# Performance work log

Hardware: AMD Instinct MI355X
Metric: run time of the kernel (lower is better)

Reference implementation:

```python
import jax, jax.numpy as jnp
import numpy as np

T, HID, HQ, HKV, D = 2048, 4096, 32, 8, 128
ROPE_BASE = 10000.0


def setup_inputs() -> dict:
    key = jax.random.key(0)
    ks = jax.random.split(key, 5)
    scale = 0.02
    hidden_states = jax.random.normal(ks[0], (T, HID), dtype=jnp.float32)
    position_ids = jnp.arange(T, dtype=jnp.int32)
    # HF-style rotary tables: freqs duplicated along last dim -> [T, D]
    inv_freq = 1.0 / (ROPE_BASE ** (jnp.arange(0, D, 2, dtype=jnp.float32) / D))
    ang = position_ids.astype(jnp.float32)[:, None] * inv_freq[None, :]  # [T, D/2]
    emb = jnp.concatenate([ang, ang], axis=-1)  # [T, D]
    cos, sin = jnp.cos(emb), jnp.sin(emb)
    Wq = jax.random.normal(ks[1], (HID, HQ * D), dtype=jnp.float32) * scale
    Wk = jax.random.normal(ks[2], (HID, HKV * D), dtype=jnp.float32) * scale
    Wv = jax.random.normal(ks[3], (HID, HKV * D), dtype=jnp.float32) * scale
    Wo = jax.random.normal(ks[4], (HQ * D, HID), dtype=jnp.float32) * scale
    return {"hidden_states": hidden_states, "position_ids": position_ids,
            "cos": cos, "sin": sin, "Wq": Wq, "Wk": Wk, "Wv": Wv, "Wo": Wo}


def _rotate_half(x):
    x1, x2 = jnp.split(x, 2, axis=-1)
    return jnp.concatenate([-x2, x1], axis=-1)


def reference(hidden_states, position_ids, cos, sin, Wq, Wk, Wv, Wo):
    t = hidden_states.shape[0]
    scaling = D ** -0.5
    # QKV projections (attention_bias=False)
    q = (hidden_states @ Wq).reshape(t, HQ, D)   # [T, Hq, D]
    k = (hidden_states @ Wk).reshape(t, HKV, D)  # [T, Hkv, D]
    v = (hidden_states @ Wv).reshape(t, HKV, D)
    # RoPE: cos/sin [T, D] broadcast over heads
    c, s = cos[:, None, :], sin[:, None, :]
    q = q * c + _rotate_half(q) * s
    k = k * c + _rotate_half(k) * s
    # GQA: expand KV heads to query heads
    groups = HQ // HKV
    k = jnp.repeat(k, groups, axis=1)  # [T, Hq, D]
    v = jnp.repeat(v, groups, axis=1)
    # Causal attention
    scores = jnp.einsum('thd,shd->hts', q, k) * scaling  # [Hq, T, T]
    causal = jnp.tril(jnp.ones((t, t), dtype=bool))
    scores = jnp.where(causal[None], scores, jnp.finfo(scores.dtype).min)
    probs = jax.nn.softmax(scores, axis=-1)
    attn = jnp.einsum('hts,shd->thd', probs, v).reshape(t, HQ * D)
    return attn @ Wo
```

## Files before the change

### kernel.cpp

```cpp
#include <hip/hip_runtime.h>
#include <hip/hip_bf16.h>
#include <cstdint>
#include <cstddef>

#define T_DIM   2048
#define HID     4096
#define HQ      32
#define HKV     8
#define D_HEAD  128
#define QKV_N   6144
#define KOFF    4096
#define VOFF    5120

typedef __attribute__((ext_vector_type(8))) short short8;
typedef __attribute__((ext_vector_type(4))) float floatx4;

__device__ __forceinline__ ushort f2bf(float f) {
    union { float f; uint u; } v; v.f = f;
    uint r = v.u + 0x7fffu + ((v.u >> 16) & 1u);
    return (ushort)(r >> 16);
}
__device__ __forceinline__ float bf2f(ushort h) {
    union { uint u; float f; } v; v.u = ((uint)h) << 16; return v.f;
}
__device__ __forceinline__ short8 ld8(const ushort* p) {
    uint2 a = *(const uint2*)p, b = *(const uint2*)(p + 4);
    union { uint u[4]; short8 s; } x;
    x.u[0] = a.x; x.u[1] = a.y; x.u[2] = b.x; x.u[3] = b.y;
    return x.s;
}
__device__ __forceinline__ void gld_lds16(const ushort* g, ushort* l) {
    __builtin_amdgcn_global_load_lds(
        (__attribute__((address_space(1))) void*)(g),
        (__attribute__((address_space(3))) void*)(l), 16, 0, 0);
}

__global__ void cast_f32_bf16(const float* __restrict__ in, ushort* __restrict__ out, int n) {
    int i = (blockIdx.x * blockDim.x + threadIdx.x) * 4;
    if (i < n) {
        float4 v = *(const float4*)(in + i);
        ushort4 o;
        o.x = f2bf(v.x); o.y = f2bf(v.y); o.z = f2bf(v.z); o.w = f2bf(v.w);
        *(ushort4*)(out + i) = o;
    }
}

__global__ __launch_bounds__(256) void transpose_cast(const float* __restrict__ W,
                                                      ushort* __restrict__ Wt, int K, int N) {
    __shared__ ushort tile[64][66];
    int n0 = blockIdx.x * 64, k0 = blockIdx.y * 64;
    int tx = threadIdx.x & 15, ty = threadIdx.x >> 4;
#pragma unroll
    for (int i = 0; i < 4; i++) {
        int r = ty + i * 16;
        float4 v = *(const float4*)&W[(size_t)(k0 + r) * N + n0 + tx * 4];
        tile[tx * 4 + 0][r] = f2bf(v.x);
        tile[tx * 4 + 1][r] = f2bf(v.y);
        tile[tx * 4 + 2][r] = f2bf(v.z);
        tile[tx * 4 + 3][r] = f2bf(v.w);
    }
    __syncthreads();
#pragma unroll
    for (int i = 0; i < 4; i++) {
        int nr = ty + i * 16;
        ushort4 o = *(const ushort4*)&tile[nr][tx * 4];
        *(ushort4*)&Wt[(size_t)(n0 + nr) * K + k0 + tx * 4] = o;
    }
}

__global__ void transpose_v(const ushort* __restrict__ qkv, ushort* __restrict__ VtG) {
    __shared__ ushort tile[32][33];
    int t0 = blockIdx.x * 32, d0 = blockIdx.y * 32, kvh = blockIdx.z;
    int tx = threadIdx.x & 31, ty = threadIdx.x >> 5;
#pragma unroll
    for (int i = 0; i < 4; i++) {
        int t = t0 + ty + i * 8;
        tile[ty + i * 8][tx] = qkv[(size_t)t * QKV_N + VOFF + kvh * D_HEAD + d0 + tx];
    }
    __syncthreads();
#pragma unroll
    for (int i = 0; i < 4; i++) {
        int d = d0 + ty + i * 8;
        VtG[((size_t)kvh * D_HEAD + d) * T_DIM + t0 + tx] = tile[tx][ty + i * 8];
    }
}

template <typename OutT>
__global__ __launch_bounds__(512, 2) void gemm256(const ushort* __restrict__ A,
                                                  const ushort* __restrict__ Bt,
                                                  OutT* __restrict__ C,
                                                  int K, int lda, int ldb, int ldc) {
    __shared__ ushort As[2][16384];
    __shared__ ushort Bs[2][16384];
    int tid = threadIdx.x;
    int wid = tid >> 6, lane = tid & 63, quad = lane >> 4, l15 = lane & 15;
    int wr = wid >> 2, wc = wid & 3;
    int bh = wc >> 1, br = (wc & 1) * 64;
    int m0 = blockIdx.x * 256, n0 = blockIdx.y * 256;
    int sw = (l15 & 7);

    floatx4 acc[8][4];
    floatx4 z = {0.f, 0.f, 0.f, 0.f};
#pragma unroll
    for (int i = 0; i < 8; i++)
#pragma unroll
        for (int j = 0; j < 4; j++) acc[i][j] = z;

    int NT = K >> 6;

    int r8 = tid >> 3;
    int csw = (tid & 7) ^ (r8 & 7);
    const ushort* sA = A  + (size_t)(m0 + r8) * lda + csw * 8;
    const ushort* sB = Bt + (size_t)(n0 + r8) * ldb + csw * 8;

    gld_lds16(sA,                          &As[0][tid * 8]);
    gld_lds16(sA + (size_t)128 * lda,      &As[0][8192 + tid * 8]);
    gld_lds16(sB,                          &Bs[0][tid * 8]);
    gld_lds16(sB + (size_t)128 * ldb,      &Bs[0][8192 + tid * 8]);
    gld_lds16(sB + (size_t)64 * ldb,       &Bs[0][4096 + tid * 8]);
    gld_lds16(sB + (size_t)192 * ldb,      &Bs[0][12288 + tid * 8]);
    gld_lds16(sA + (size_t)64 * lda,       &As[0][4096 + tid * 8]);
    gld_lds16(sA + (size_t)192 * lda,      &As[0][12288 + tid * 8]);
    asm volatile("s_waitcnt vmcnt(2)" ::: "memory");
    __builtin_amdgcn_sched_barrier(0);
    __builtin_amdgcn_s_barrier();

    short8 bfr[4][2];
    short8 af[2][2];

    for (int t = 0; t < NT; ++t) {
        int slot = t & 1, ns = slot ^ 1;
        const ushort* tA = &As[slot][wr * 8192];
        const ushort* tB = &Bs[slot][bh * 8192];
        size_t ko = (size_t)(t + 1) * 64;
        bool pf = (t + 1 < NT);

#pragma unroll
        for (int nf = 0; nf < 4; ++nf)
#pragma unroll
            for (int kh = 0; kh < 2; ++kh)
                bfr[nf][kh] = *(const short8*)&tB[(br + nf * 16 + l15) * 64 +
                                                  (((quad + kh * 4) ^ sw) * 8)];
#pragma unroll
        for (int mi = 0; mi < 2; ++mi)
#pragma unroll
            for (int kh = 0; kh < 2; ++kh)
                af[mi][kh] = *(const short8*)&tA[(mi * 16 + l15) * 64 +
                                                 (((quad + kh * 4) ^ sw) * 8)];
        if (pf) {
            gld_lds16(sA + ko,                     &As[ns][tid * 8]);
            gld_lds16(sA + (size_t)128 * lda + ko, &As[ns][8192 + tid * 8]);
        }
        __builtin_amdgcn_sched_barrier(0);
        __builtin_amdgcn_s_barrier();
        asm volatile("s_waitcnt lgkmcnt(0)" ::: "memory");
        __builtin_amdgcn_sched_barrier(0);
        __builtin_amdgcn_s_setprio(1);
#pragma unroll
        for (int nf = 0; nf < 4; ++nf)
#pragma unroll
            for (int mi = 0; mi < 2; ++mi)
#pragma unroll
                for (int kh = 0; kh < 2; ++kh)
                    acc[mi][nf] = __builtin_amdgcn_mfma_f32_16x16x32_bf16(af[mi][kh], bfr[nf][kh], acc[mi][nf], 0, 0, 0);
        __builtin_amdgcn_s_setprio(0);
        __builtin_amdgcn_sched_barrier(0);
        __builtin_amdgcn_s_barrier();

#pragma unroll
        for (int mi = 0; mi < 2; ++mi)
#pragma unroll
            for (int kh = 0; kh < 2; ++kh)
                af[mi][kh] = *(const short8*)&tA[(32 + mi * 16 + l15) * 64 +
                                                 (((quad + kh * 4) ^ sw) * 8)];
        if (pf) {
            gld_lds16(sB + ko,                     &Bs[ns][tid * 8]);
            gld_lds16(sB + (size_t)128 * ldb + ko, &Bs[ns][8192 + tid * 8]);
        }
        __builtin_amdgcn_sched_barrier(0);
        __builtin_amdgcn_s_barrier();
        asm volatile("s_waitcnt lgkmcnt(0)" ::: "memory");
        __builtin_amdgcn_sched_barrier(0);
        __builtin_amdgcn_s_setprio(1);
#pragma unroll
        for (int nf = 0; nf < 4; ++nf)
#pragma unroll
            for (int mi = 0; mi < 2; ++mi)
#pragma unroll
                for (int kh = 0; kh < 2; ++kh)
                    acc[2 + mi][nf] = __builtin_amdgcn_mfma_f32_16x16x32_bf16(af[mi][kh], bfr[nf][kh], acc[2 + mi][nf], 0, 0, 0);
        __builtin_amdgcn_s_setprio(0);
        __builtin_amdgcn_sched_barrier(0);
        if (pf) asm volatile("s_waitcnt vmcnt(4)" ::: "memory");
        else    asm volatile("s_waitcnt vmcnt(0)" ::: "memory");
        __builtin_amdgcn_sched_barrier(0);
        __builtin_amdgcn_s_barrier();

#pragma unroll
        for (int mi = 0; mi < 2; ++mi)
#pragma unroll
            for (int kh = 0; kh < 2; ++kh)
                af[mi][kh] = *(const short8*)&tA[(64 + mi * 16 + l15) * 64 +
                                                 (((quad + kh * 4) ^ sw) * 8)];
        if (pf) {
            gld_lds16(sB + (size_t)64 * ldb + ko,  &Bs[ns][4096 + tid * 8]);
            gld_lds16(sB + (size_t)192 * ldb + ko, &Bs[ns][12288 + tid * 8]);
        }
        __builtin_amdgcn_sched_barrier(0);
        __builtin_amdgcn_s_barrier();
        asm volatile("s_waitcnt lgkmcnt(0)" ::: "memory");
        __builtin_amdgcn_sched_barrier(0);
        __builtin_amdgcn_s_setprio(1);
#pragma unroll
        for (int nf = 0; nf < 4; ++nf)
#pragma unroll
            for (int mi = 0; mi < 2; ++mi)
#pragma unroll
                for (int kh = 0; kh < 2; ++kh)
                    acc[4 + mi][nf] = __builtin_amdgcn_mfma_f32_16x16x32_bf16(af[mi][kh], bfr[nf][kh], acc[4 + mi][nf], 0, 0, 0);
        __builtin_amdgcn_s_setprio(0);
        __builtin_amdgcn_sched_barrier(0);
        __builtin_amdgcn_s_barrier();

#pragma unroll
        for (int mi = 0; mi < 2; ++mi)
#pragma unroll
            for (int kh = 0; kh < 2; ++kh)
                af[mi][kh] = *(const short8*)&tA[(96 + mi * 16 + l15) * 64 +
                                                 (((quad + kh * 4) ^ sw) * 8)];
        if (pf) {
            gld_lds16(sA + (size_t)64 * lda + ko,  &As[ns][4096 + tid * 8]);
            gld_lds16(sA + (size_t)192 * lda + ko, &As[ns][12288 + tid * 8]);
        }
        __builtin_amdgcn_sched_barrier(0);
        __builtin_amdgcn_s_barrier();
        asm volatile("s_waitcnt lgkmcnt(0)" ::: "memory");
        __builtin_amdgcn_sched_barrier(0);
        __builtin_amdgcn_s_setprio(1);
#pragma unroll
        for (int nf = 0; nf < 4; ++nf)
#pragma unroll
            for (int mi = 0; mi < 2; ++mi)
#pragma unroll
                for (int kh = 0; kh < 2; ++kh)
                    acc[6 + mi][nf] = __builtin_amdgcn_mfma_f32_16x16x32_bf16(af[mi][kh], bfr[nf][kh], acc[6 + mi][nf], 0, 0, 0);
        __builtin_amdgcn_s_setprio(0);
        __builtin_amdgcn_sched_barrier(0);
        if (pf) asm volatile("s_waitcnt vmcnt(2)" ::: "memory");
        __builtin_amdgcn_sched_barrier(0);
        __builtin_amdgcn_s_barrier();
    }

#pragma unroll
    for (int i = 0; i < 8; ++i) {
        int row0 = m0 + wr * 128 + i * 16 + quad * 4;
#pragma unroll
        for (int j = 0; j < 4; ++j) {
            int col = n0 + wc * 64 + j * 16 + l15;
#pragma unroll
            for (int r = 0; r < 4; ++r) {
                float v = acc[i][j][r];
                if constexpr (sizeof(OutT) == 2)
                    C[(size_t)(row0 + r) * ldc + col] = (OutT)f2bf(v);
                else
                    C[(size_t)(row0 + r) * ldc + col] = v;
            }
        }
    }
}

template <typename OutT>
__global__ __launch_bounds__(256) void gemm_bt(const ushort* __restrict__ A,
                                               const ushort* __restrict__ Bt,
                                               OutT* __restrict__ C,
                                               int K, int lda, int ldb, int ldc) {
    __shared__ ushort As[2][128 * 32];
    __shared__ ushort Bs[2][128 * 32];
    int tid = threadIdx.x;
    int w = tid >> 6, lane = tid & 63, quad = lane >> 4, l15 = lane & 15;
    int wr = (w >> 1) * 64, wc = (w & 1) * 64;
    int m0 = blockIdx.x * 128, n0 = blockIdx.y * 128;

    floatx4 acc[4][4];
    floatx4 z = {0.f, 0.f, 0.f, 0.f};
#pragma unroll
    for (int i = 0; i < 4; i++)
#pragma unroll
        for (int j = 0; j < 4; j++) acc[i][j] = z;

    int arow = tid >> 2, ac = (tid & 3) * 8;
    const ushort* gA0 = A + (size_t)(m0 + arow) * lda + ac;
    const ushort* gA1 = A + (size_t)(m0 + arow + 64) * lda + ac;
    const ushort* gB0 = Bt + (size_t)(n0 + arow) * ldb + ac;
    const ushort* gB1 = Bt + (size_t)(n0 + arow + 64) * ldb + ac;

    gld_lds16(gA0, &As[0][tid * 8]);
    gld_lds16(gA1, &As[0][64 * 32 + tid * 8]);
    gld_lds16(gB0, &Bs[0][tid * 8]);
    gld_lds16(gB1, &Bs[0][64 * 32 + tid * 8]);
    gA0 += 32; gA1 += 32; gB0 += 32; gB1 += 32;

    int cur = 0;
    for (int k0 = 0; k0 < K; k0 += 32, cur ^= 1) {
        __syncthreads();
        if (k0 + 32 < K) {
            gld_lds16(gA0, &As[cur ^ 1][tid * 8]);
            gld_lds16(gA1, &As[cur ^ 1][64 * 32 + tid * 8]);
            gld_lds16(gB0, &Bs[cur ^ 1][tid * 8]);
            gld_lds16(gB1, &Bs[cur ^ 1][64 * 32 + tid * 8]);
            gA0 += 32; gA1 += 32; gB0 += 32; gB1 += 32;
        }

        short8 af[4];
#pragma unroll
        for (int i = 0; i < 4; i++)
            af[i] = *(const short8*)&As[cur][(wr + i * 16 + l15) * 32 + quad * 8];
#pragma unroll
        for (int j = 0; j < 4; j++) {
            short8 bf = *(const short8*)&Bs[cur][(wc + j * 16 + l15) * 32 + quad * 8];
#pragma unroll
            for (int i = 0; i < 4; i++)
                acc[i][j] = __builtin_amdgcn_mfma_f32_16x16x32_bf16(af[i], bf, acc[i][j], 0, 0, 0);
        }
    }

#pragma unroll
    for (int i = 0; i < 4; i++) {
        int row0 = m0 + wr + i * 16 + quad * 4;
#pragma unroll
        for (int j = 0; j < 4; j++) {
            int col = n0 + wc + j * 16 + l15;
#pragma unroll
            for (int r = 0; r < 4; r++) {
                float v = acc[i][j][r];
                if constexpr (sizeof(OutT) == 2)
                    C[(size_t)(row0 + r) * ldc + col] = (OutT)f2bf(v);
                else
                    C[(size_t)(row0 + r) * ldc + col] = v;
            }
        }
    }
}

__global__ void rope_kernel(ushort* __restrict__ qkv, const float* __restrict__ cosb,
                            const float* __restrict__ sinb) {
    int t = blockIdx.x;
    ushort* row = qkv + (size_t)t * QKV_N;
    const float* cr = cosb + (size_t)t * D_HEAD;
    const float* sr = sinb + (size_t)t * D_HEAD;
    for (int c = threadIdx.x; c < 2560; c += 256) {
        int slice = c >> 6, d = c & 63;
        int col = slice * 128 + d;
        float x0 = bf2f(row[col]), x1 = bf2f(row[col + 64]);
        float cs = cr[d], sn = sr[d];
        row[col] = f2bf(x0 * cs - x1 * sn);
        row[col + 64] = f2bf(x1 * cs + x0 * sn);
    }
}

#define PS_STRIDE 68

__global__ __launch_bounds__(256, 2) void attn_kernel(const ushort* __restrict__ qkv,
                                                      const ushort* __restrict__ VtG,
                                                      ushort* __restrict__ attn) {
    __shared__ ushort Ks[64 * 128];
    __shared__ ushort Vt[128 * 64];
    __shared__ ushort Ps[128 * PS_STRIDE];

    int qt = (gridDim.x - 1) - blockIdx.x;
    int h = blockIdx.y;
    int q0 = qt * 128;
    int kbmax = 2 * qt + 1;
    int tid = threadIdx.x, w = tid >> 6, lane = tid & 63, quad = lane >> 4, l15 = lane & 15;
    int kvh = h >> 2;

    const ushort* kbase = qkv + (size_t)KOFF + (size_t)kvh * D_HEAD;
    const ushort* vbase = VtG + (size_t)kvh * D_HEAD * T_DIM;

    const ushort* ksrc[4];
    const ushort* vsrc[4];
#pragma unroll
    for (int i = 0; i < 4; i++) {
        int cid = i * 256 + tid;
        int kr = cid >> 4, kp = cid & 15, kc = kp ^ (kr & 15);
        ksrc[i] = kbase + (size_t)kr * QKV_N + kc * 8;
        int vr = cid >> 3, vp = cid & 7, vc = vp ^ (vr & 7);
        vsrc[i] = vbase + (size_t)vr * T_DIM + vc * 8;
    }

#pragma unroll
    for (int i = 0; i < 4; i++) {
        gld_lds16(ksrc[i], &Ks[(i * 256 + tid) * 8]);
        ksrc[i] += (size_t)64 * QKV_N;
    }

    short8 qf[2][4];
#pragma unroll
    for (int s = 0; s < 2; s++) {
        const ushort* qrow = qkv + (size_t)(q0 + s * 64 + w * 16 + l15) * QKV_N + h * D_HEAD + quad * 8;
#pragma unroll
        for (int ks = 0; ks < 4; ks++)
            qf[s][ks] = *(const short8*)(qrow + ks * 32);
    }

    floatx4 o[2][8];
    floatx4 z = {0.f, 0.f, 0.f, 0.f};
#pragma unroll
    for (int s = 0; s < 2; s++)
#pragma unroll
        for (int j = 0; j < 8; j++) o[s][j] = z;
    float lsum[2][4] = {{0.f, 0.f, 0.f, 0.f}, {0.f, 0.f, 0.f, 0.f}};

    const float scale_l2e = 0.08838834764831845f * 1.4426950408889634f;
    const float BOUND = 24.0f;

    __syncthreads();

    for (int kb = 0; kb <= kbmax; kb++) {
        bool act0 = (kb <= 2 * qt);

#pragma unroll
        for (int i = 0; i < 4; i++) {
            gld_lds16(vsrc[i], &Vt[(i * 256 + tid) * 8]);
            vsrc[i] += 64;
        }

        floatx4 sc[2][4];
#pragma unroll
        for (int s = 0; s < 2; s++)
#pragma unroll
            for (int jt = 0; jt < 4; jt++) sc[s][jt] = z;
#pragma unroll
        for (int ks = 0; ks < 4; ks++) {
#pragma unroll
            for (int jt = 0; jt < 4; jt++) {
                short8 kf = ld8(&Ks[(jt * 16 + l15) * 128 + (((ks * 4 + quad) ^ l15) * 8)]);
                if (act0)
                    sc[0][jt] = __builtin_amdgcn_mfma_f32_16x16x32_bf16(qf[0][ks], kf, sc[0][jt], 0, 0, 0);
                sc[1][jt] = __builtin_amdgcn_mfma_f32_16x16x32_bf16(qf[1][ks], kf, sc[1][jt], 0, 0, 0);
            }
        }

#pragma unroll
        for (int s = 0; s < 2; s++) {
            if (s == 0 && !act0) continue;
            bool diag = (kb == 2 * qt + s);
#pragma unroll
            for (int r = 0; r < 4; r++) {
                int rloc = w * 16 + quad * 4 + r;
#pragma unroll
                for (int jt = 0; jt < 4; jt++) {
                    float v = fmaf(sc[s][jt][r], scale_l2e, -BOUND);
                    if (diag && (jt * 16 + l15 > rloc)) v = -1e30f;
                    float p = exp2f(v);
                    lsum[s][r] += p;
                    Ps[(s * 64 + rloc) * PS_STRIDE + jt * 16 + l15] = f2bf(p);
                }
            }
        }

        __syncthreads();

        if (kb < kbmax) {
#pragma unroll
            for (int i = 0; i < 4; i++) {
                gld_lds16(ksrc[i], &Ks[(i * 256 + tid) * 8]);
                ksrc[i] += (size_t)64 * QKV_N;
            }
        }

#pragma unroll
        for (int ks2 = 0; ks2 < 2; ks2++) {
            short8 pf0 = ld8(&Ps[(w * 16 + l15) * PS_STRIDE + ks2 * 32 + quad * 8]);
            short8 pf1 = ld8(&Ps[(64 + w * 16 + l15) * PS_STRIDE + ks2 * 32 + quad * 8]);
#pragma unroll
            for (int jt = 0; jt < 8; jt++) {
                short8 vf = ld8(&Vt[(jt * 16 + l15) * 64 + (((ks2 * 4 + quad) ^ (l15 & 7)) * 8)]);
                if (act0)
                    o[0][jt] = __builtin_amdgcn_mfma_f32_16x16x32_bf16(pf0, vf, o[0][jt], 0, 0, 0);
                o[1][jt] = __builtin_amdgcn_mfma_f32_16x16x32_bf16(pf1, vf, o[1][jt], 0, 0, 0);
            }
        }

        __syncthreads();
    }

#pragma unroll
    for (int s = 0; s < 2; s++) {
#pragma unroll
        for (int r = 0; r < 4; r++) {
            float l = lsum[s][r];
#pragma unroll
            for (int mk = 1; mk <= 8; mk <<= 1) l += __shfl_xor(l, mk);
            float inv = 1.f / l;
            int trow = q0 + s * 64 + w * 16 + quad * 4 + r;
            ushort* orow = attn + (size_t)trow * (HQ * D_HEAD) + h * D_HEAD;
#pragma unroll
            for (int jt = 0; jt < 8; jt++)
                orow[jt * 16 + l15] = f2bf(o[s][jt][r] * inv);
        }
    }
}

extern "C" void kernel_launch(void* const* d_in, const int* in_sizes, int n_in,
                              void* d_out, int out_size, void* d_ws, size_t ws_size,
                              hipStream_t stream) {
    const float* hidden = (const float*)d_in[0];
    const float* cosb = (const float*)d_in[2];
    const float* sinb = (const float*)d_in[3];
    const float* Wq = (const float*)d_in[4];
    const float* Wk = (const float*)d_in[5];
    const float* Wv = (const float*)d_in[6];
    const float* Wo = (const float*)d_in[7];
    float* out = (float*)d_out;

    char* ws = (char*)d_ws;
    ushort* hiddenB = (ushort*)(ws);
    ushort* WqkvT   = (ushort*)(ws + (size_t)(16u << 20));
    ushort* WoT     = (ushort*)(ws + (size_t)(64u << 20));
    ushort* qkv     = (ushort*)(ws + (size_t)(96u << 20));
    ushort* attnO   = (ushort*)(ws + (size_t)(120u << 20));
    ushort* VtG     = (ushort*)(ws + (size_t)(136u << 20));

    cast_f32_bf16<<<8192, 256, 0, stream>>>(hidden, hiddenB, T_DIM * HID);
    transpose_cast<<<dim3(64, 64), 256, 0, stream>>>(Wq, WqkvT, HID, 4096);
    transpose_cast<<<dim3(16, 64), 256, 0, stream>>>(Wk, WqkvT + (size_t)4096 * HID, HID, 1024);
    transpose_cast<<<dim3(16, 64), 256, 0, stream>>>(Wv, WqkvT + (size_t)5120 * HID, HID, 1024);
    transpose_cast<<<dim3(64, 64), 256, 0, stream>>>(Wo, WoT, HID, 4096);

    gemm256<ushort><<<dim3(8, 24), 512, 0, stream>>>(hiddenB, WqkvT, qkv,
                                                     HID, HID, HID, QKV_N);
    rope_kernel<<<T_DIM, 256, 0, stream>>>(qkv, cosb, sinb);
    transpose_v<<<dim3(64, 4, 8), 256, 0, stream>>>(qkv, VtG);
    attn_kernel<<<dim3(T_DIM / 128, HQ), 256, 0, stream>>>(qkv, VtG, attnO);
    gemm_bt<float><<<dim3(16, 32), 256, 0, stream>>>(attnO, WoT, out,
                                                     HID, HID, HID, HID);
}
```

Baseline: 569.8 us.

## Retile QKV and output GEMMs for full CU coverage, vectorize rope and transpose

```diff
diff --git a/kernel.cpp b/kernel.cpp
--- a/kernel.cpp
+++ b/kernel.cpp
@@ -47,7 +47,7 @@
 
 __global__ __launch_bounds__(256) void transpose_cast(const float* __restrict__ W,
                                                       ushort* __restrict__ Wt, int K, int N) {
-    __shared__ ushort tile[64][66];
+    __shared__ ushort tile[64][72];
     int n0 = blockIdx.x * 64, k0 = blockIdx.y * 64;
     int tx = threadIdx.x & 15, ty = threadIdx.x >> 4;
 #pragma unroll
@@ -61,10 +61,11 @@
     }
     __syncthreads();
 #pragma unroll
-    for (int i = 0; i < 4; i++) {
-        int nr = ty + i * 16;
-        ushort4 o = *(const ushort4*)&tile[nr][tx * 4];
-        *(ushort4*)&Wt[(size_t)(n0 + nr) * K + k0 + tx * 4] = o;
+    for (int i = 0; i < 2; i++) {
+        int task = i * 256 + threadIdx.x;
+        int nr = task >> 3, c = task & 7;
+        short8 o = *(const short8*)&tile[nr][c * 8];
+        *(short8*)&Wt[(size_t)(n0 + nr) * K + k0 + c * 8] = o;
     }
 }
 
@@ -85,71 +86,67 @@
     }
 }
 
-template <typename OutT>
-__global__ __launch_bounds__(512, 2) void gemm256(const ushort* __restrict__ A,
-                                                  const ushort* __restrict__ Bt,
-                                                  OutT* __restrict__ C,
-                                                  int K, int lda, int ldb, int ldc) {
+__global__ __launch_bounds__(512, 1) void gemm_qkv(const ushort* __restrict__ A,
+                                                   const ushort* __restrict__ Bt,
+                                                   ushort* __restrict__ C,
+                                                   int K, int lda, int ldb, int ldc) {
     __shared__ ushort As[2][16384];
-    __shared__ ushort Bs[2][16384];
+    __shared__ ushort Bs[2][12288];
     int tid = threadIdx.x;
     int wid = tid >> 6, lane = tid & 63, quad = lane >> 4, l15 = lane & 15;
     int wr = wid >> 2, wc = wid & 3;
-    int bh = wc >> 1, br = (wc & 1) * 64;
-    int m0 = blockIdx.x * 256, n0 = blockIdx.y * 256;
-    int sw = (l15 & 7);
-
-    floatx4 acc[8][4];
+    int m0 = blockIdx.x * 256, n0 = blockIdx.y * 192;
+    int sw = l15 & 7;
+
+    floatx4 acc[8][3];
     floatx4 z = {0.f, 0.f, 0.f, 0.f};
 #pragma unroll
     for (int i = 0; i < 8; i++)
 #pragma unroll
-        for (int j = 0; j < 4; j++) acc[i][j] = z;
+        for (int j = 0; j < 3; j++) acc[i][j] = z;
 
     int NT = K >> 6;
-
     int r8 = tid >> 3;
     int csw = (tid & 7) ^ (r8 & 7);
-    const ushort* sA = A  + (size_t)(m0 + r8) * lda + csw * 8;
+    const ushort* sA = A + (size_t)(m0 + r8) * lda + csw * 8;
     const ushort* sB = Bt + (size_t)(n0 + r8) * ldb + csw * 8;
 
-    gld_lds16(sA,                          &As[0][tid * 8]);
-    gld_lds16(sA + (size_t)128 * lda,      &As[0][8192 + tid * 8]);
-    gld_lds16(sB,                          &Bs[0][tid * 8]);
-    gld_lds16(sB + (size_t)128 * ldb,      &Bs[0][8192 + tid * 8]);
-    gld_lds16(sB + (size_t)64 * ldb,       &Bs[0][4096 + tid * 8]);
-    gld_lds16(sB + (size_t)192 * ldb,      &Bs[0][12288 + tid * 8]);
-    gld_lds16(sA + (size_t)64 * lda,       &As[0][4096 + tid * 8]);
-    gld_lds16(sA + (size_t)192 * lda,      &As[0][12288 + tid * 8]);
+    gld_lds16(sB,                      &Bs[0][tid * 8]);
+    gld_lds16(sB + (size_t)64 * ldb,   &Bs[0][4096 + tid * 8]);
+    gld_lds16(sB + (size_t)128 * ldb,  &Bs[0][8192 + tid * 8]);
+    gld_lds16(sA,                      &As[0][tid * 8]);
+    gld_lds16(sA + (size_t)128 * lda,  &As[0][8192 + tid * 8]);
+    gld_lds16(sA + (size_t)64 * lda,   &As[0][4096 + tid * 8]);
+    gld_lds16(sA + (size_t)192 * lda,  &As[0][12288 + tid * 8]);
     asm volatile("s_waitcnt vmcnt(2)" ::: "memory");
     __builtin_amdgcn_sched_barrier(0);
     __builtin_amdgcn_s_barrier();
 
-    short8 bfr[4][2];
+    short8 bfr[3][2];
     short8 af[2][2];
 
     for (int t = 0; t < NT; ++t) {
         int slot = t & 1, ns = slot ^ 1;
-        const ushort* tA = &As[slot][wr * 8192];
-        const ushort* tB = &Bs[slot][bh * 8192];
+        const ushort* tA = &As[slot][0];
+        const ushort* tB = &Bs[slot][0];
         size_t ko = (size_t)(t + 1) * 64;
         bool pf = (t + 1 < NT);
 
 #pragma unroll
-        for (int nf = 0; nf < 4; ++nf)
-#pragma unroll
-            for (int kh = 0; kh < 2; ++kh)
-                bfr[nf][kh] = *(const short8*)&tB[(br + nf * 16 + l15) * 64 +
+        for (int nf = 0; nf < 3; ++nf)
+#pragma unroll
+            for (int kh = 0; kh < 2; ++kh)
+                bfr[nf][kh] = *(const short8*)&tB[(wc * 48 + nf * 16 + l15) * 64 +
                                                   (((quad + kh * 4) ^ sw) * 8)];
 #pragma unroll
         for (int mi = 0; mi < 2; ++mi)
 #pragma unroll
             for (int kh = 0; kh < 2; ++kh)
-                af[mi][kh] = *(const short8*)&tA[(mi * 16 + l15) * 64 +
+                af[mi][kh] = *(const short8*)&tA[(wr * 128 + mi * 16 + l15) * 64 +
                                                  (((quad + kh * 4) ^ sw) * 8)];
         if (pf) {
-            gld_lds16(sA + ko,                     &As[ns][tid * 8]);
-            gld_lds16(sA + (size_t)128 * lda + ko, &As[ns][8192 + tid * 8]);
+            gld_lds16(sB + ko,                    &Bs[ns][tid * 8]);
+            gld_lds16(sB + (size_t)64 * ldb + ko, &Bs[ns][4096 + tid * 8]);
         }
         __builtin_amdgcn_sched_barrier(0);
         __builtin_amdgcn_s_barrier();
@@ -157,7 +154,7 @@
         __builtin_amdgcn_sched_barrier(0);
         __builtin_amdgcn_s_setprio(1);
 #pragma unroll
-        for (int nf = 0; nf < 4; ++nf)
+        for (int nf = 0; nf < 3; ++nf)
 #pragma unroll
             for (int mi = 0; mi < 2; ++mi)
 #pragma unroll
@@ -171,11 +168,11 @@
         for (int mi = 0; mi < 2; ++mi)
 #pragma unroll
             for (int kh = 0; kh < 2; ++kh)
-                af[mi][kh] = *(const short8*)&tA[(32 + mi * 16 + l15) * 64 +
+                af[mi][kh] = *(const short8*)&tA[(wr * 128 + 32 + mi * 16 + l15) * 64 +
                                                  (((quad + kh * 4) ^ sw) * 8)];
         if (pf) {
-            gld_lds16(sB + ko,                     &Bs[ns][tid * 8]);
             gld_lds16(sB + (size_t)128 * ldb + ko, &Bs[ns][8192 + tid * 8]);
+            gld_lds16(sA + ko,                     &As[ns][tid * 8]);
         }
         __builtin_amdgcn_sched_barrier(0);
         __builtin_amdgcn_s_barrier();
@@ -183,7 +180,7 @@
         __builtin_amdgcn_sched_barrier(0);
         __builtin_amdgcn_s_setprio(1);
 #pragma unroll
-        for (int nf = 0; nf < 4; ++nf)
+        for (int nf = 0; nf < 3; ++nf)
 #pragma unroll
             for (int mi = 0; mi < 2; ++mi)
 #pragma unroll
@@ -200,11 +197,10 @@
         for (int mi = 0; mi < 2; ++mi)
 #pragma unroll
             for (int kh = 0; kh < 2; ++kh)
-                af[mi][kh] = *(const short8*)&tA[(64 + mi * 16 + l15) * 64 +
+                af[mi][kh] = *(const short8*)&tA[(wr * 128 + 64 + mi * 16 + l15) * 64 +
                                                  (((quad + kh * 4) ^ sw) * 8)];
         if (pf) {
-            gld_lds16(sB + (size_t)64 * ldb + ko,  &Bs[ns][4096 + tid * 8]);
-            gld_lds16(sB + (size_t)192 * ldb + ko, &Bs[ns][12288 + tid * 8]);
+            gld_lds16(sA + (size_t)128 * lda + ko, &As[ns][8192 + tid * 8]);
         }
         __builtin_amdgcn_sched_barrier(0);
         __builtin_amdgcn_s_barrier();
@@ -212,7 +208,7 @@
         __builtin_amdgcn_sched_barrier(0);
         __builtin_amdgcn_s_setprio(1);
 #pragma unroll
-        for (int nf = 0; nf < 4; ++nf)
+        for (int nf = 0; nf < 3; ++nf)
 #pragma unroll
             for (int mi = 0; mi < 2; ++mi)
 #pragma unroll
@@ -226,7 +222,7 @@
         for (int mi = 0; mi < 2; ++mi)
 #pragma unroll
             for (int kh = 0; kh < 2; ++kh)
-                af[mi][kh] = *(const short8*)&tA[(96 + mi * 16 + l15) * 64 +
+                af[mi][kh] = *(const short8*)&tA[(wr * 128 + 96 + mi * 16 + l15) * 64 +
                                                  (((quad + kh * 4) ^ sw) * 8)];
         if (pf) {
             gld_lds16(sA + (size_t)64 * lda + ko,  &As[ns][4096 + tid * 8]);
@@ -238,7 +234,7 @@
         __builtin_amdgcn_sched_barrier(0);
         __builtin_amdgcn_s_setprio(1);
 #pragma unroll
-        for (int nf = 0; nf < 4; ++nf)
+        for (int nf = 0; nf < 3; ++nf)
 #pragma unroll
             for (int mi = 0; mi < 2; ++mi)
 #pragma unroll
@@ -255,107 +251,166 @@
     for (int i = 0; i < 8; ++i) {
         int row0 = m0 + wr * 128 + i * 16 + quad * 4;
 #pragma unroll
-        for (int j = 0; j < 4; ++j) {
-            int col = n0 + wc * 64 + j * 16 + l15;
-#pragma unroll
-            for (int r = 0; r < 4; ++r) {
-                float v = acc[i][j][r];
-                if constexpr (sizeof(OutT) == 2)
-                    C[(size_t)(row0 + r) * ldc + col] = (OutT)f2bf(v);
-                else
-                    C[(size_t)(row0 + r) * ldc + col] = v;
-            }
-        }
-    }
-}
-
-template <typename OutT>
-__global__ __launch_bounds__(256) void gemm_bt(const ushort* __restrict__ A,
-                                               const ushort* __restrict__ Bt,
-                                               OutT* __restrict__ C,
-                                               int K, int lda, int ldb, int ldc) {
-    __shared__ ushort As[2][128 * 32];
-    __shared__ ushort Bs[2][128 * 32];
+        for (int j = 0; j < 3; ++j) {
+            int col = n0 + wc * 48 + j * 16 + l15;
+#pragma unroll
+            for (int r = 0; r < 4; ++r)
+                C[(size_t)(row0 + r) * ldc + col] = f2bf(acc[i][j][r]);
+        }
+    }
+}
+
+__global__ __launch_bounds__(512, 1) void gemm_out(const ushort* __restrict__ A,
+                                                   const ushort* __restrict__ Bt,
+                                                   float* __restrict__ C,
+                                                   int K, int lda, int ldb, int ldc) {
+    __shared__ ushort As[2][16384];
+    __shared__ ushort Bs[2][8192];
     int tid = threadIdx.x;
-    int w = tid >> 6, lane = tid & 63, quad = lane >> 4, l15 = lane & 15;
-    int wr = (w >> 1) * 64, wc = (w & 1) * 64;
-    int m0 = blockIdx.x * 128, n0 = blockIdx.y * 128;
-
-    floatx4 acc[4][4];
+    int wid = tid >> 6, lane = tid & 63, quad = lane >> 4, l15 = lane & 15;
+    int wr = wid >> 2, wc = wid & 3;
+    int m0 = blockIdx.x * 256, n0 = blockIdx.y * 128;
+    int sw = l15 & 7;
+
+    floatx4 acc[8][2];
     floatx4 z = {0.f, 0.f, 0.f, 0.f};
 #pragma unroll
-    for (int i = 0; i < 4; i++)
-#pragma unroll
-        for (int j = 0; j < 4; j++) acc[i][j] = z;
-
-    int arow = tid >> 2, ac = (tid & 3) * 8;
-    const ushort* gA0 = A + (size_t)(m0 + arow) * lda + ac;
-    const ushort* gA1 = A + (size_t)(m0 + arow + 64) * lda + ac;
-    const ushort* gB0 = Bt + (size_t)(n0 + arow) * ldb + ac;
-    const ushort* gB1 = Bt + (size_t)(n0 + arow + 64) * ldb + ac;
-
-    gld_lds16(gA0, &As[0][tid * 8]);
-    gld_lds16(gA1, &As[0][64 * 32 + tid * 8]);
-    gld_lds16(gB0, &Bs[0][tid * 8]);
-    gld_lds16(gB1, &Bs[0][64 * 32 + tid * 8]);
-    gA0 += 32; gA1 += 32; gB0 += 32; gB1 += 32;
-
-    int cur = 0;
-    for (int k0 = 0; k0 < K; k0 += 32, cur ^= 1) {
-        __syncthreads();
-        if (k0 + 32 < K) {
-            gld_lds16(gA0, &As[cur ^ 1][tid * 8]);
-            gld_lds16(gA1, &As[cur ^ 1][64 * 32 + tid * 8]);
-            gld_lds16(gB0, &Bs[cur ^ 1][tid * 8]);
-            gld_lds16(gB1, &Bs[cur ^ 1][64 * 32 + tid * 8]);
-            gA0 += 32; gA1 += 32; gB0 += 32; gB1 += 32;
-        }
-
-        short8 af[4];
-#pragma unroll
-        for (int i = 0; i < 4; i++)
-            af[i] = *(const short8*)&As[cur][(wr + i * 16 + l15) * 32 + quad * 8];
-#pragma unroll
-        for (int j = 0; j < 4; j++) {
-            short8 bf = *(const short8*)&Bs[cur][(wc + j * 16 + l15) * 32 + quad * 8];
-#pragma unroll
-            for (int i = 0; i < 4; i++)
-                acc[i][j] = __builtin_amdgcn_mfma_f32_16x16x32_bf16(af[i], bf, acc[i][j], 0, 0, 0);
-        }
-    }
-
-#pragma unroll
-    for (int i = 0; i < 4; i++) {
-        int row0 = m0 + wr + i * 16 + quad * 4;
-#pragma unroll
-        for (int j = 0; j < 4; j++) {
-            int col = n0 + wc + j * 16 + l15;
-#pragma unroll
-            for (int r = 0; r < 4; r++) {
-                float v = acc[i][j][r];
-                if constexpr (sizeof(OutT) == 2)
-                    C[(size_t)(row0 + r) * ldc + col] = (OutT)f2bf(v);
-                else
-                    C[(size_t)(row0 + r) * ldc + col] = v;
-            }
-        }
-    }
-}
-
-__global__ void rope_kernel(ushort* __restrict__ qkv, const float* __restrict__ cosb,
-                            const float* __restrict__ sinb) {
+    for (int i = 0; i < 8; i++)
+#pragma unroll
+        for (int j = 0; j < 2; j++) acc[i][j] = z;
+
+    int NT = K >> 6;
+    int r8 = tid >> 3;
+    int csw = (tid & 7) ^ (r8 & 7);
+    const ushort* sA = A + (size_t)(m0 + r8) * lda + csw * 8;
+    const ushort* sB = Bt + (size_t)(n0 + r8) * ldb + csw * 8;
+
+    gld_lds16(sB,                      &Bs[0][tid * 8]);
+    gld_lds16(sB + (size_t)64 * ldb,   &Bs[0][4096 + tid * 8]);
+    gld_lds16(sA,                      &As[0][tid * 8]);
+    gld_lds16(sA + (size_t)128 * lda,  &As[0][8192 + tid * 8]);
+    gld_lds16(sA + (size_t)64 * lda,   &As[0][4096 + tid * 8]);
+    gld_lds16(sA + (size_t)192 * lda,  &As[0][12288 + tid * 8]);
+    asm volatile("s_waitcnt vmcnt(2)" ::: "memory");
+    __builtin_amdgcn_sched_barrier(0);
+    __builtin_amdgcn_s_barrier();
+
+    short8 bfr[2][2];
+    short8 af[4][2];
+
+    for (int t = 0; t < NT; ++t) {
+        int slot = t & 1, ns = slot ^ 1;
+        const ushort* tA = &As[slot][0];
+        const ushort* tB = &Bs[slot][0];
+        size_t ko = (size_t)(t + 1) * 64;
+        bool pf = (t + 1 < NT);
+
+#pragma unroll
+        for (int nf = 0; nf < 2; ++nf)
+#pragma unroll
+            for (int kh = 0; kh < 2; ++kh)
+                bfr[nf][kh] = *(const short8*)&tB[(wc * 32 + nf * 16 + l15) * 64 +
+                                                  (((quad + kh * 4) ^ sw) * 8)];
+#pragma unroll
+        for (int mi = 0; mi < 4; ++mi)
+#pragma unroll
+            for (int kh = 0; kh < 2; ++kh)
+                af[mi][kh] = *(const short8*)&tA[(wr * 128 + mi * 16 + l15) * 64 +
+                                                 (((quad + kh * 4) ^ sw) * 8)];
+        if (pf) {
+            gld_lds16(sB + ko,                    &Bs[ns][tid * 8]);
+            gld_lds16(sB + (size_t)64 * ldb + ko, &Bs[ns][4096 + tid * 8]);
+            gld_lds16(sA + ko,                    &As[ns][tid * 8]);
+        }
+        __builtin_amdgcn_sched_barrier(0);
+        __builtin_amdgcn_s_barrier();
+        asm volatile("s_waitcnt lgkmcnt(0)" ::: "memory");
+        __builtin_amdgcn_sched_barrier(0);
+        __builtin_amdgcn_s_setprio(1);
+#pragma unroll
+        for (int nf = 0; nf < 2; ++nf)
+#pragma unroll
+            for (int mi = 0; mi < 4; ++mi)
+#pragma unroll
+                for (int kh = 0; kh < 2; ++kh)
+                    acc[mi][nf] = __builtin_amdgcn_mfma_f32_16x16x32_bf16(af[mi][kh], bfr[nf][kh], acc[mi][nf], 0, 0, 0);
+        __builtin_amdgcn_s_setprio(0);
+        __builtin_amdgcn_sched_barrier(0);
+        if (pf) asm volatile("s_waitcnt vmcnt(3)" ::: "memory");
+        else    asm volatile("s_waitcnt vmcnt(0)" ::: "memory");
+        __builtin_amdgcn_sched_barrier(0);
+        __builtin_amdgcn_s_barrier();
+
+#pragma unroll
+        for (int mi = 0; mi < 4; ++mi)
+#pragma unroll
+            for (int kh = 0; kh < 2; ++kh)
+                af[mi][kh] = *(const short8*)&tA[(wr * 128 + 64 + mi * 16 + l15) * 64 +
+                                                 (((quad + kh * 4) ^ sw) * 8)];
+        if (pf) {
+            gld_lds16(sA + (size_t)128 * lda + ko, &As[ns][8192 + tid * 8]);
+            gld_lds16(sA + (size_t)64 * lda + ko,  &As[ns][4096 + tid * 8]);
+            gld_lds16(sA + (size_t)192 * lda + ko, &As[ns][12288 + tid * 8]);
+        }
+        __builtin_amdgcn_sched_barrier(0);
+        __builtin_amdgcn_s_barrier();
+        asm volatile("s_waitcnt lgkmcnt(0)" ::: "memory");
+        __builtin_amdgcn_sched_barrier(0);
+        __builtin_amdgcn_s_setprio(1);
+#pragma unroll
+        for (int nf = 0; nf < 2; ++nf)
+#pragma unroll
+            for (int mi = 0; mi < 4; ++mi)
+#pragma unroll
+                for (int kh = 0; kh < 2; ++kh)
+                    acc[4 + mi][nf] = __builtin_amdgcn_mfma_f32_16x16x32_bf16(af[mi][kh], bfr[nf][kh], acc[4 + mi][nf], 0, 0, 0);
+        __builtin_amdgcn_s_setprio(0);
+        __builtin_amdgcn_sched_barrier(0);
+        if (pf) asm volatile("s_waitcnt vmcnt(2)" ::: "memory");
+        __builtin_amdgcn_sched_barrier(0);
+        __builtin_amdgcn_s_barrier();
+    }
+
+#pragma unroll
+    for (int i = 0; i < 8; ++i) {
+        int row0 = m0 + wr * 128 + i * 16 + quad * 4;
+#pragma unroll
+        for (int j = 0; j < 2; ++j) {
+            int col = n0 + wc * 32 + j * 16 + l15;
+#pragma unroll
+            for (int r = 0; r < 4; ++r)
+                C[(size_t)(row0 + r) * ldc + col] = acc[i][j][r];
+        }
+    }
+}
+
+__global__ __launch_bounds__(320) void rope_kernel(ushort* __restrict__ qkv,
+                                                   const float* __restrict__ cosb,
+                                                   const float* __restrict__ sinb) {
     int t = blockIdx.x;
     ushort* row = qkv + (size_t)t * QKV_N;
     const float* cr = cosb + (size_t)t * D_HEAD;
     const float* sr = sinb + (size_t)t * D_HEAD;
-    for (int c = threadIdx.x; c < 2560; c += 256) {
-        int slice = c >> 6, d = c & 63;
-        int col = slice * 128 + d;
-        float x0 = bf2f(row[col]), x1 = bf2f(row[col + 64]);
-        float cs = cr[d], sn = sr[d];
-        row[col] = f2bf(x0 * cs - x1 * sn);
-        row[col + 64] = f2bf(x1 * cs + x0 * sn);
-    }
+    int task = threadIdx.x;
+    int slice = task >> 3, d8 = (task & 7) * 8;
+    int col = slice * 128 + d8;
+    short8 a = *(const short8*)&row[col];
+    short8 b = *(const short8*)&row[col + 64];
+    float4 c0 = *(const float4*)&cr[d8], c1 = *(const float4*)&cr[d8 + 4];
+    float4 s0 = *(const float4*)&sr[d8], s1 = *(const float4*)&sr[d8 + 4];
+    short8 oa, ob;
+#pragma unroll
+    for (int j = 0; j < 8; j++) {
+        float cs = (j < 4) ? ((j == 0) ? c0.x : (j == 1) ? c0.y : (j == 2) ? c0.z : c0.w)
+                           : ((j == 4) ? c1.x : (j == 5) ? c1.y : (j == 6) ? c1.z : c1.w);
+        float sn = (j < 4) ? ((j == 0) ? s0.x : (j == 1) ? s0.y : (j == 2) ? s0.z : s0.w)
+                           : ((j == 4) ? s1.x : (j == 5) ? s1.y : (j == 6) ? s1.z : s1.w);
+        float x0 = bf2f((ushort)a[j]), x1 = bf2f((ushort)b[j]);
+        oa[j] = (short)f2bf(x0 * cs - x1 * sn);
+        ob[j] = (short)f2bf(x1 * cs + x0 * sn);
+    }
+    *(short8*)&row[col] = oa;
+    *(short8*)&row[col + 64] = ob;
 }
 
 #define PS_STRIDE 68
@@ -528,11 +583,9 @@
     transpose_cast<<<dim3(16, 64), 256, 0, stream>>>(Wv, WqkvT + (size_t)5120 * HID, HID, 1024);
     transpose_cast<<<dim3(64, 64), 256, 0, stream>>>(Wo, WoT, HID, 4096);
 
-    gemm256<ushort><<<dim3(8, 24), 512, 0, stream>>>(hiddenB, WqkvT, qkv,
-                                                     HID, HID, HID, QKV_N);
-    rope_kernel<<<T_DIM, 256, 0, stream>>>(qkv, cosb, sinb);
+    gemm_qkv<<<dim3(8, 32), 512, 0, stream>>>(hiddenB, WqkvT, qkv, HID, HID, HID, QKV_N);
+    rope_kernel<<<T_DIM, 320, 0, stream>>>(qkv, cosb, sinb);
     transpose_v<<<dim3(64, 4, 8), 256, 0, stream>>>(qkv, VtG);
     attn_kernel<<<dim3(T_DIM / 128, HQ), 256, 0, stream>>>(qkv, VtG, attnO);
-    gemm_bt<float><<<dim3(16, 32), 256, 0, stream>>>(attnO, WoT, out,
-                                                     HID, HID, HID, HID);
-}
+    gemm_out<<<dim3(8, 32), 512, 0, stream>>>(attnO, WoT, out, HID, HID, HID, HID);
+}
```

Measured after the change: 558.6 us. No clear change (-2.0%).
